# Kernel tuning notes

Measured on AMD Instinct MI355X. Metric: run time of the kernel, lower is better.

## Reference

```python
import jax, jax.numpy as jnp
import numpy as np

N = 50000
E = 800000
R = 5
D = 128
Q = D // 4  # 32


def setup_inputs() -> dict:
    key = jax.random.key(0)
    ks = jax.random.split(key, 24)
    s = 0.05
    inp = {
        'des': jax.random.normal(ks[0], (N, 768), jnp.float32),
        'tweet': jax.random.normal(ks[1], (N, 768), jnp.float32),
        'num_prop': jax.random.normal(ks[2], (N, 6), jnp.float32),
        'cat_prop': jax.random.normal(ks[3], (N, 11), jnp.float32),
        'edge_index': jax.random.randint(ks[4], (2, E), 0, N, dtype=jnp.int32),
        'edge_type': jax.random.randint(ks[5], (E,), 0, R, dtype=jnp.int32),
        'W_des': jax.random.normal(ks[6], (768, Q), jnp.float32) * s,
        'b_des': jnp.zeros((Q,), jnp.float32),
        'W_tw': jax.random.normal(ks[7], (768, Q), jnp.float32) * s,
        'b_tw': jnp.zeros((Q,), jnp.float32),
        'W_np': jax.random.normal(ks[8], (6, Q), jnp.float32) * s,
        'b_np': jnp.zeros((Q,), jnp.float32),
        'W_cp': jax.random.normal(ks[9], (11, Q), jnp.float32) * s,
        'b_cp': jnp.zeros((Q,), jnp.float32),
        'W_in': jax.random.normal(ks[10], (D, D), jnp.float32) * s,
        'b_in': jnp.zeros((D,), jnp.float32),
        'rel_w': jax.random.normal(ks[11], (R, D, D), jnp.float32) * s,
        'root_w': jax.random.normal(ks[12], (D, D), jnp.float32) * s,
        'rgcn_b': jnp.zeros((D,), jnp.float32),
        'W_o1': jax.random.normal(ks[13], (D, D), jnp.float32) * s,
        'b_o1': jnp.zeros((D,), jnp.float32),
        'W_o2': jax.random.normal(ks[14], (D, 2), jnp.float32) * s,
        'b_o2': jnp.zeros((2,), jnp.float32),
    }
    return inp


def _lrelu(v):
    return jax.nn.leaky_relu(v, negative_slope=0.01)


def _rgcn(x, edge_index, edge_type, rel_w, root_w, rgcn_b):
    # PyG RGCNConv with default mean aggregation per relation.
    n = x.shape[0]
    src, dst = edge_index[0], edge_index[1]
    h = jnp.einsum('nd,rde->rne', x, rel_w)          # [R, N, D]
    msg = h[edge_type, src]                          # [E, D] gather per edge
    seg = dst * R + edge_type                        # combined (node, relation) key
    sums = jax.ops.segment_sum(msg, seg, num_segments=n * R).reshape(n, R, -1)
    cnt = jax.ops.segment_sum(jnp.ones(msg.shape[0], jnp.float32), seg,
                              num_segments=n * R).reshape(n, R, 1)
    agg = (sums / jnp.maximum(cnt, 1.0)).sum(axis=1)  # mean per relation, sum over relations
    return agg + x @ root_w + rgcn_b


def reference(des, tweet, num_prop, cat_prop, edge_index, edge_type,
              W_des, b_des, W_tw, b_tw, W_np, b_np, W_cp, b_cp,
              W_in, b_in, rel_w, root_w, rgcn_b, W_o1, b_o1, W_o2, b_o2):
    d = _lrelu(des @ W_des + b_des)
    t = _lrelu(tweet @ W_tw + b_tw)
    n_ = _lrelu(num_prop @ W_np + b_np)
    c = _lrelu(cat_prop @ W_cp + b_cp)
    x = jnp.concatenate([d, t, n_, c], axis=1)       # [N, D]
    x = _lrelu(x @ W_in + b_in)
    for _ in range(4):
        x = _rgcn(x, edge_index, edge_type, rel_w, root_w, rgcn_b)
    x = _lrelu(x @ W_o1 + b_o1)
    return x @ W_o2 + b_o2                            # [N, 2]
```

## Files before the change

kernel.cpp:

```cpp
#include <hip/hip_runtime.h>


#define N_NODES 50000
#define N_EDGES 800000
#define R_REL   5
#define NSEG    (N_NODES * R_REL)
#define SCAN_BS 1024
#define SCAN_NB ((NSEG + SCAN_BS - 1) / SCAN_BS)

typedef __attribute__((ext_vector_type(8))) short bf16x8;
typedef __attribute__((ext_vector_type(4))) float f32x4;

__device__ __forceinline__ float lrelu(float v) { return v > 0.f ? v : 0.01f * v; }

__device__ __forceinline__ unsigned short f2bf_rne(float f) {
    unsigned u = __float_as_uint(f);
    return (unsigned short)((u + 0x7fff + ((u >> 16) & 1)) >> 16);
}

__device__ __forceinline__ void split1(float f, short& h, short& l) {
    unsigned u = __float_as_uint(f);
    unsigned short hh = (unsigned short)(u >> 16);
    h = (short)hh;
    l = (short)f2bf_rne(f - __uint_as_float((unsigned)hh << 16));
}

__device__ __forceinline__ void split8(const float* f, bf16x8& hi, bf16x8& lo) {
#pragma unroll
    for (int i = 0; i < 8; i++) {
        short h, l;
        split1(f[i], h, l);
        hi[i] = h;
        lo[i] = l;
    }
}

__global__ __launch_bounds__(256) void count_kernel(const int* __restrict__ ei,
                                                    const int* __restrict__ et,
                                                    int* __restrict__ cnt) {
    int e = blockIdx.x * 256 + threadIdx.x;
    if (e >= N_EDGES) return;
    atomicAdd(&cnt[ei[N_EDGES + e] * R_REL + et[e]], 1);
}

__global__ __launch_bounds__(SCAN_BS) void scan1(const int* __restrict__ cnt,
                                                 int* __restrict__ rowptr,
                                                 int* __restrict__ blockSums) {
    __shared__ int s[SCAN_BS];
    int t = threadIdx.x;
    int i = blockIdx.x * SCAN_BS + t;
    int v = (i < NSEG) ? cnt[i] : 0;
    s[t] = v;
    __syncthreads();
#pragma unroll
    for (int off = 1; off < SCAN_BS; off <<= 1) {
        int add = (t >= off) ? s[t - off] : 0;
        __syncthreads();
        s[t] += add;
        __syncthreads();
    }
    if (i < NSEG) rowptr[i] = s[t] - v;
    if (t == SCAN_BS - 1) blockSums[blockIdx.x] = s[t];
}

__global__ __launch_bounds__(256) void scan2(int* __restrict__ blockSums) {
    __shared__ int s[256];
    int t = threadIdx.x;
    int v = (t < SCAN_NB) ? blockSums[t] : 0;
    s[t] = v;
    __syncthreads();
#pragma unroll
    for (int off = 1; off < 256; off <<= 1) {
        int add = (t >= off) ? s[t - off] : 0;
        __syncthreads();
        s[t] += add;
        __syncthreads();
    }
    if (t < SCAN_NB) blockSums[t] = s[t] - v;
}

__global__ __launch_bounds__(SCAN_BS) void scan3(int* __restrict__ rowptr,
                                                 const int* __restrict__ blockSums) {
    int i = blockIdx.x * SCAN_BS + threadIdx.x;
    if (i == 0) rowptr[NSEG] = N_EDGES;
    if (i < NSEG) rowptr[i] += blockSums[blockIdx.x];
}

__global__ __launch_bounds__(256) void fill_kernel(const int* __restrict__ ei,
                                                   const int* __restrict__ et,
                                                   const int* __restrict__ rowptr,
                                                   int* __restrict__ cursor,
                                                   int* __restrict__ srcSorted) {
    int e = blockIdx.x * 256 + threadIdx.x;
    if (e >= N_EDGES) return;
    int seg = ei[N_EDGES + e] * R_REL + et[e];
    int pos = atomicAdd(&cursor[seg], 1);
    srcSorted[rowptr[seg] + pos] = ei[e];
}

__global__ __launch_bounds__(256) void build_bswz(const float* __restrict__ W,
                                                  int K, int NC, int NTILES,
                                                  short* __restrict__ out) {
    int tid = blockIdx.x * 256 + threadIdx.x;
    int total = (K / 32) * NTILES * 64;
    if (tid >= total) return;
    int l  = tid & 63;
    int nt = (tid >> 6) % NTILES;
    int c  = tid / (64 * NTILES);
    int n = nt * 16 + (l & 15);
    int k0 = c * 32 + (l >> 4) * 8;
    float f[8];
#pragma unroll
    for (int j = 0; j < 8; j++) f[j] = W[(size_t)(k0 + j) * NC + n];
    bf16x8 hi, lo;
    split8(f, hi, lo);
    size_t base = (size_t)c * (2 * NTILES * 512);
    *(bf16x8*)(out + base + ((size_t)nt * 64 + l) * 8) = hi;
    *(bf16x8*)(out + base + (size_t)NTILES * 512 + ((size_t)nt * 64 + l) * 8) = lo;
}

__global__ __launch_bounds__(256, 5) void rgcn_fused(const float* __restrict__ xf,
                                                     const int* __restrict__ rowptr,
                                                     const int* __restrict__ srcSorted,
                                                     const short* __restrict__ bz,
                                                     const float* __restrict__ rgcn_b,
                                                     float* __restrict__ xn, int M) {
    __shared__ short AhS[4][2048];
    __shared__ short AlS[4][2048];
    const int t = threadIdx.x;
    const int m0 = blockIdx.x * 64;
    const int w = t >> 6, l = t & 63;
    const int q = l >> 4, ln = l & 15;
    const int mw = w >> 1, nw = w & 1;
    const int rr = w * 16 + (t & 15);
    const int qq = (t >> 4) & 3;
    const int node = m0 + rr;
    const int sidx = w * 512 + l * 8;

    f32x4 acc[2][4];
#pragma unroll
    for (int mt = 0; mt < 2; mt++)
#pragma unroll
        for (int nt = 0; nt < 4; nt++) acc[mt][nt] = (f32x4)0.f;

    auto AGG = [&](int rel) {
        float ag[4][8];
#pragma unroll
        for (int c = 0; c < 4; c++)
#pragma unroll
            for (int j = 0; j < 8; j++) ag[c][j] = 0.f;
        int beg = 0, end = 0;
        if (node < M) {
            int s = node * R_REL + rel;
            beg = rowptr[s];
            end = rowptr[s + 1];
        }
        int i = beg;
        for (; i + 1 < end; i += 2) {
            int s0 = srcSorted[i];
            int s1 = srcSorted[i + 1];
            const float* p0 = xf + (size_t)s0 * 128 + qq * 8;
            const float* p1 = xf + (size_t)s1 * 128 + qq * 8;
#pragma unroll
            for (int c = 0; c < 4; c++) {
                float4 a0 = *(const float4*)(p0 + c * 32);
                float4 a1 = *(const float4*)(p0 + c * 32 + 4);
                float4 b0 = *(const float4*)(p1 + c * 32);
                float4 b1 = *(const float4*)(p1 + c * 32 + 4);
                ag[c][0] += a0.x + b0.x; ag[c][1] += a0.y + b0.y;
                ag[c][2] += a0.z + b0.z; ag[c][3] += a0.w + b0.w;
                ag[c][4] += a1.x + b1.x; ag[c][5] += a1.y + b1.y;
                ag[c][6] += a1.z + b1.z; ag[c][7] += a1.w + b1.w;
            }
        }
        if (i < end) {
            int s0 = srcSorted[i];
            const float* p0 = xf + (size_t)s0 * 128 + qq * 8;
#pragma unroll
            for (int c = 0; c < 4; c++) {
                float4 a0 = *(const float4*)(p0 + c * 32);
                float4 a1 = *(const float4*)(p0 + c * 32 + 4);
                ag[c][0] += a0.x; ag[c][1] += a0.y; ag[c][2] += a0.z; ag[c][3] += a0.w;
                ag[c][4] += a1.x; ag[c][5] += a1.y; ag[c][6] += a1.z; ag[c][7] += a1.w;
            }
        }
        int cnum = end - beg;
        float inv = cnum > 0 ? 1.f / (float)cnum : 0.f;
#pragma unroll
        for (int c = 0; c < 4; c++) {
            bf16x8 hv, lv;
#pragma unroll
            for (int j = 0; j < 8; j++) {
                short hh, ll;
                split1(ag[c][j] * inv, hh, ll);
                hv[j] = hh; lv[j] = ll;
            }
            *(bf16x8*)&AhS[c][sidx] = hv;
            *(bf16x8*)&AlS[c][sidx] = lv;
        }
    };

    auto ROOT = [&]() {
        int gr = node < M ? node : M - 1;
        const float* p0 = xf + (size_t)gr * 128 + qq * 8;
#pragma unroll
        for (int c = 0; c < 4; c++) {
            float f[8];
            *(float4*)&f[0] = *(const float4*)(p0 + c * 32);
            *(float4*)&f[4] = *(const float4*)(p0 + c * 32 + 4);
            bf16x8 hv, lv;
            split8(f, hv, lv);
            *(bf16x8*)&AhS[c][sidx] = hv;
            *(bf16x8*)&AlS[c][sidx] = lv;
        }
    };

    auto GEMMP = [&](const short* bzr) {
        bf16x8 BH[2][4], BL[2][4];
#pragma unroll
        for (int nt = 0; nt < 4; nt++) {
            const short* bp = bzr + (nw * 4 + nt) * 512 + l * 8;
            BH[0][nt] = *(const bf16x8*)(bp);
            BL[0][nt] = *(const bf16x8*)(bp + 4096);
        }
#pragma unroll
        for (int c = 0; c < 4; c++) {
            if (c < 3) {
#pragma unroll
                for (int nt = 0; nt < 4; nt++) {
                    const short* bp = bzr + (c + 1) * 8192 + (nw * 4 + nt) * 512 + l * 8;
                    BH[(c + 1) & 1][nt] = *(const bf16x8*)(bp);
                    BL[(c + 1) & 1][nt] = *(const bf16x8*)(bp + 4096);
                }
            }
            bf16x8 ah[2], al[2];
#pragma unroll
            for (int mt = 0; mt < 2; mt++) {
                ah[mt] = *(const bf16x8*)&AhS[c][(mw * 2 + mt) * 512 + l * 8];
                al[mt] = *(const bf16x8*)&AlS[c][(mw * 2 + mt) * 512 + l * 8];
            }
#pragma unroll
            for (int nt = 0; nt < 4; nt++) {
                bf16x8 bh = BH[c & 1][nt];
                bf16x8 bl2 = BL[c & 1][nt];
#pragma unroll
                for (int mt = 0; mt < 2; mt++) {
                    acc[mt][nt] = __builtin_amdgcn_mfma_f32_16x16x32_bf16(ah[mt], bh, acc[mt][nt], 0, 0, 0);
                    acc[mt][nt] = __builtin_amdgcn_mfma_f32_16x16x32_bf16(ah[mt], bl2, acc[mt][nt], 0, 0, 0);
                    acc[mt][nt] = __builtin_amdgcn_mfma_f32_16x16x32_bf16(al[mt], bh, acc[mt][nt], 0, 0, 0);
                }
            }
        }
    };

#pragma unroll 1
    for (int r = 0; r < 6; r++) {
        if (r > 0) __syncthreads();
        if (r < 5) AGG(r); else ROOT();
        __syncthreads();
        GEMMP(bz + (size_t)r * 32768);
    }

#pragma unroll
    for (int nt = 0; nt < 4; nt++) {
        int col = (nw * 4 + nt) * 16 + ln;
        float bv = rgcn_b[col];
#pragma unroll
        for (int mt = 0; mt < 2; mt++) {
            f32x4 v = acc[mt][nt];
#pragma unroll
            for (int i = 0; i < 4; i++) {
                int m = m0 + (mw * 2 + mt) * 16 + q * 4 + i;
                if (m < M) xn[(size_t)m * 128 + col] = v[i] + bv;
            }
        }
    }
}

template <int NT, bool ACT>
__global__ __launch_bounds__(256) void mfma_gemm(const float* __restrict__ A, int K,
                                                 const short* __restrict__ Bswz,
                                                 const float* __restrict__ bias,
                                                 float* __restrict__ C, int M,
                                                 int colofs) {
    constexpr int NH = NT / 2;
    __shared__ short Ahi[2048], Alo[2048];
    __shared__ short Bs[NT * 1024];
    const int t = threadIdx.x;
    const int m0 = blockIdx.x * 64;
    const int w = t >> 6, l = t & 63;
    const int q = l >> 4, ln = l & 15;
    const int mw = w >> 1, nw = w & 1;

    f32x4 acc[2][NH];
#pragma unroll
    for (int mt = 0; mt < 2; mt++)
#pragma unroll
        for (int nt = 0; nt < NH; nt++) acc[mt][nt] = (f32x4)0.f;

    const int nchunks = K / 32;
    const int r = t >> 2, qq = t & 3;
    const int aidx = (r >> 4) * 512 + qq * 128 + (r & 15) * 8;
    int gr = m0 + r; if (gr >= M) gr = M - 1;

    for (int c = 0; c < nchunks; c++) {
        __syncthreads();
        {
            const float* ap = A + (size_t)gr * K + c * 32 + qq * 8;
            float f[8];
            *(float4*)&f[0] = ((const float4*)ap)[0];
            *(float4*)&f[4] = ((const float4*)ap)[1];
            bf16x8 h0, l0;
            split8(f, h0, l0);
            *(bf16x8*)&Ahi[aidx] = h0;
            *(bf16x8*)&Alo[aidx] = l0;
        }
        {
            const short* gb = Bswz + (size_t)c * (NT * 1024);
#pragma unroll
            for (int i = 0; i < NH; i++) {
                int idx = i * 256 + t;
                *(bf16x8*)&Bs[idx * 8] = *(const bf16x8*)(gb + (size_t)idx * 8);
            }
        }
        __syncthreads();

        bf16x8 a_hi[2], a_lo[2];
#pragma unroll
        for (int mt = 0; mt < 2; mt++) {
            a_hi[mt] = *(const bf16x8*)&Ahi[(mw * 2 + mt) * 512 + l * 8];
            a_lo[mt] = *(const bf16x8*)&Alo[(mw * 2 + mt) * 512 + l * 8];
        }
#pragma unroll
        for (int nt = 0; nt < NH; nt++) {
            int ng = nw * NH + nt;
            bf16x8 bh = *(const bf16x8*)&Bs[(ng * 64 + l) * 8];
            bf16x8 bl = *(const bf16x8*)&Bs[NT * 512 + (ng * 64 + l) * 8];
#pragma unroll
            for (int mt = 0; mt < 2; mt++) {
                acc[mt][nt] = __builtin_amdgcn_mfma_f32_16x16x32_bf16(a_hi[mt], bh, acc[mt][nt], 0, 0, 0);
                acc[mt][nt] = __builtin_amdgcn_mfma_f32_16x16x32_bf16(a_hi[mt], bl, acc[mt][nt], 0, 0, 0);
                acc[mt][nt] = __builtin_amdgcn_mfma_f32_16x16x32_bf16(a_lo[mt], bh, acc[mt][nt], 0, 0, 0);
            }
        }
    }

#pragma unroll
    for (int nt = 0; nt < NH; nt++) {
        int ng = nw * NH + nt;
        int col = colofs + ng * 16 + ln;
        float bv = bias[ng * 16 + ln];
#pragma unroll
        for (int mt = 0; mt < 2; mt++) {
            f32x4 v = acc[mt][nt];
#pragma unroll
            for (int i = 0; i < 4; i++) {
                int m = m0 + (mw * 2 + mt) * 16 + q * 4 + i;
                if (m < M) {
                    float xv = v[i] + bv;
                    if (ACT) xv = lrelu(xv);
                    C[(size_t)m * 128 + col] = xv;
                }
            }
        }
    }
}

__global__ __launch_bounds__(256) void encode_small(const float* __restrict__ num_prop,
                                                    const float* __restrict__ cat_prop,
                                                    const float* __restrict__ W_np,
                                                    const float* __restrict__ b_np,
                                                    const float* __restrict__ W_cp,
                                                    const float* __restrict__ b_cp,
                                                    float* __restrict__ x) {
    int t = blockIdx.x * 256 + threadIdx.x;
    int node = t >> 6;
    int jj = t & 63;
    if (node >= N_NODES) return;
    if (jj < 32) {
        float acc = b_np[jj];
        const float* row = num_prop + (size_t)node * 6;
#pragma unroll
        for (int k = 0; k < 6; k++) acc = fmaf(row[k], W_np[k * 32 + jj], acc);
        x[(size_t)node * 128 + 64 + jj] = lrelu(acc);
    } else {
        int j = jj - 32;
        float acc = b_cp[j];
        const float* row = cat_prop + (size_t)node * 11;
#pragma unroll
        for (int k = 0; k < 11; k++) acc = fmaf(row[k], W_cp[k * 32 + j], acc);
        x[(size_t)node * 128 + 96 + j] = lrelu(acc);
    }
}

__global__ __launch_bounds__(256) void out_proj(const float* __restrict__ X,
                                                const float* __restrict__ W,
                                                const float* __restrict__ b,
                                                float* __restrict__ out, int M) {
    int n = blockIdx.x * 256 + threadIdx.x;
    if (n >= M) return;
    float a0 = b[0], a1 = b[1];
    const float4* xr = (const float4*)(X + (size_t)n * 128);
#pragma unroll
    for (int k4 = 0; k4 < 32; k4++) {
        float4 v = xr[k4];
        a0 = fmaf(v.x, W[(k4 * 4 + 0) * 2 + 0], a0);
        a1 = fmaf(v.x, W[(k4 * 4 + 0) * 2 + 1], a1);
        a0 = fmaf(v.y, W[(k4 * 4 + 1) * 2 + 0], a0);
        a1 = fmaf(v.y, W[(k4 * 4 + 1) * 2 + 1], a1);
        a0 = fmaf(v.z, W[(k4 * 4 + 2) * 2 + 0], a0);
        a1 = fmaf(v.z, W[(k4 * 4 + 2) * 2 + 1], a1);
        a0 = fmaf(v.w, W[(k4 * 4 + 3) * 2 + 0], a0);
        a1 = fmaf(v.w, W[(k4 * 4 + 3) * 2 + 1], a1);
    }
    out[(size_t)n * 2 + 0] = a0;
    out[(size_t)n * 2 + 1] = a1;
}

static inline size_t align64(size_t x) { return (x + 63) & ~(size_t)63; }

extern "C" void kernel_launch(void* const* d_in, const int* in_sizes, int n_in,
                              void* d_out, int out_size, void* d_ws, size_t ws_size,
                              hipStream_t stream) {
    const float* des      = (const float*)d_in[0];
    const float* tweet    = (const float*)d_in[1];
    const float* num_prop = (const float*)d_in[2];
    const float* cat_prop = (const float*)d_in[3];
    const int*   edge_index = (const int*)d_in[4];
    const int*   edge_type  = (const int*)d_in[5];
    const float* W_des = (const float*)d_in[6];  const float* b_des = (const float*)d_in[7];
    const float* W_tw  = (const float*)d_in[8];  const float* b_tw  = (const float*)d_in[9];
    const float* W_np  = (const float*)d_in[10]; const float* b_np  = (const float*)d_in[11];
    const float* W_cp  = (const float*)d_in[12]; const float* b_cp  = (const float*)d_in[13];
    const float* W_in  = (const float*)d_in[14]; const float* b_in  = (const float*)d_in[15];
    const float* rel_w = (const float*)d_in[16]; const float* root_w = (const float*)d_in[17];
    const float* rgcn_b = (const float*)d_in[18];
    const float* W_o1  = (const float*)d_in[19]; const float* b_o1  = (const float*)d_in[20];
    const float* W_o2  = (const float*)d_in[21]; const float* b_o2  = (const float*)d_in[22];
    float* out = (float*)d_out;

    char* p = (char*)d_ws;
    float* xA  = (float*)p;            p += (size_t)N_NODES * 128 * 4;
    float* xB  = (float*)p;            p += (size_t)N_NODES * 128 * 4;
    int* cnt       = (int*)p;          p += (size_t)NSEG * 4;
    int* rowptr    = (int*)p;          p += (size_t)(NSEG + 1) * 4;
    int* cursor    = (int*)p;          p += (size_t)NSEG * 4;
    int* srcSorted = (int*)p;          p += (size_t)N_EDGES * 4;
    int* blockSums = (int*)p;          p += (size_t)256 * 4;
    p = (char*)align64((size_t)p);
    short* bz_cat = (short*)p;         p += (size_t)6 * 32768 * 2;
    short* bz_in  = (short*)p;         p += (size_t)32768 * 2;
    short* bz_o1  = (short*)p;         p += (size_t)32768 * 2;
    short* bz_des = (short*)p;         p += (size_t)24 * 2048 * 2;
    short* bz_tw  = (short*)p;         p += (size_t)24 * 2048 * 2;

    for (int r = 0; r < R_REL; r++)
        build_bswz<<<8, 256, 0, stream>>>(rel_w + (size_t)r * 128 * 128, 128, 128, 8,
                                          bz_cat + (size_t)r * 32768);
    build_bswz<<<8, 256, 0, stream>>>(root_w, 128, 128, 8, bz_cat + (size_t)5 * 32768);
    build_bswz<<<8, 256, 0, stream>>>(W_in, 128, 128, 8, bz_in);
    build_bswz<<<8, 256, 0, stream>>>(W_o1, 128, 128, 8, bz_o1);
    build_bswz<<<12, 256, 0, stream>>>(W_des, 768, 32, 2, bz_des);
    build_bswz<<<12, 256, 0, stream>>>(W_tw, 768, 32, 2, bz_tw);

    hipMemsetAsync(cnt, 0, (size_t)NSEG * sizeof(int), stream);
    hipMemsetAsync(cursor, 0, (size_t)NSEG * sizeof(int), stream);
    count_kernel<<<(N_EDGES + 255) / 256, 256, 0, stream>>>(edge_index, edge_type, cnt);
    scan1<<<SCAN_NB, SCAN_BS, 0, stream>>>(cnt, rowptr, blockSums);
    scan2<<<1, 256, 0, stream>>>(blockSums);
    scan3<<<SCAN_NB, SCAN_BS, 0, stream>>>(rowptr, blockSums);
    fill_kernel<<<(N_EDGES + 255) / 256, 256, 0, stream>>>(
        edge_index, edge_type, rowptr, cursor, srcSorted);

    const int gm = (N_NODES + 63) / 64;

    encode_small<<<(N_NODES * 64 + 255) / 256, 256, 0, stream>>>(
        num_prop, cat_prop, W_np, b_np, W_cp, b_cp, xA);
    mfma_gemm<2, true><<<gm, 256, 0, stream>>>(des, 768, bz_des, b_des, xA, N_NODES, 0);
    mfma_gemm<2, true><<<gm, 256, 0, stream>>>(tweet, 768, bz_tw, b_tw, xA, N_NODES, 32);

    mfma_gemm<8, true><<<gm, 256, 0, stream>>>(xA, 128, bz_in, b_in, xB, N_NODES, 0);

    float* cur = xB; float* nxt = xA;
    for (int lyr = 0; lyr < 4; lyr++) {
        rgcn_fused<<<gm, 256, 0, stream>>>(cur, rowptr, srcSorted, bz_cat, rgcn_b, nxt, N_NODES);
        float* tmp = cur; cur = nxt; nxt = tmp;
    }

    mfma_gemm<8, true><<<gm, 256, 0, stream>>>(cur, 128, bz_o1, b_o1, nxt, N_NODES, 0);
    out_proj<<<(N_NODES + 255) / 256, 256, 0, stream>>>(nxt, W_o2, b_o2, out, N_NODES);
}
```

Measured before the change: 1.042 ms.

## Halve RGCN node tile to 32 and stage output through shared memory

```diff
diff --git a/kernel.cpp b/kernel.cpp
--- a/kernel.cpp
+++ b/kernel.cpp
@@ -119,36 +119,48 @@
     *(bf16x8*)(out + base + (size_t)NTILES * 512 + ((size_t)nt * 64 + l) * 8) = lo;
 }
 
-__global__ __launch_bounds__(256, 5) void rgcn_fused(const float* __restrict__ xf,
+__global__ __launch_bounds__(256, 6) void rgcn_fused(const float* __restrict__ xf,
                                                      const int* __restrict__ rowptr,
                                                      const int* __restrict__ srcSorted,
                                                      const short* __restrict__ bz,
                                                      const float* __restrict__ rgcn_b,
                                                      float* __restrict__ xn, int M) {
-    __shared__ short AhS[4][2048];
-    __shared__ short AlS[4][2048];
+    __shared__ __align__(16) char smem[16384];
+    short* AhS = (short*)smem;
+    short* AlS = (short*)(smem + 8192);
+    float* Co  = (float*)smem;
+
     const int t = threadIdx.x;
-    const int m0 = blockIdx.x * 64;
+    const int m0 = blockIdx.x * 32;
     const int w = t >> 6, l = t & 63;
     const int q = l >> 4, ln = l & 15;
     const int mw = w >> 1, nw = w & 1;
-    const int rr = w * 16 + (t & 15);
-    const int qq = (t >> 4) & 3;
+
+    const int rr = t & 31;
+    const int q8 = t >> 5;
     const int node = m0 + rr;
-    const int sidx = w * 512 + l * 8;
-
-    f32x4 acc[2][4];
-#pragma unroll
-    for (int mt = 0; mt < 2; mt++)
-#pragma unroll
-        for (int nt = 0; nt < 4; nt++) acc[mt][nt] = (f32x4)0.f;
+    const int cch = q8 >> 1;
+    const int kq0 = (q8 & 1) * 2;
+    const int sidx = cch * 1024 + (rr >> 4) * 512 + (kq0 * 16 + (rr & 15)) * 8;
+
+    f32x4 acc[4];
+#pragma unroll
+    for (int nt = 0; nt < 4; nt++) acc[nt] = (f32x4)0.f;
+
+    auto STAGE = [&](const float* ag) {
+        bf16x8 hv, lv;
+        split8(ag, hv, lv);
+        *(bf16x8*)&AhS[sidx] = hv;
+        *(bf16x8*)&AlS[sidx] = lv;
+        split8(ag + 8, hv, lv);
+        *(bf16x8*)&AhS[sidx + 128] = hv;
+        *(bf16x8*)&AlS[sidx + 128] = lv;
+    };
 
     auto AGG = [&](int rel) {
-        float ag[4][8];
-#pragma unroll
-        for (int c = 0; c < 4; c++)
-#pragma unroll
-            for (int j = 0; j < 8; j++) ag[c][j] = 0.f;
+        float ag[16];
+#pragma unroll
+        for (int j = 0; j < 16; j++) ag[j] = 0.f;
         int beg = 0, end = 0;
         if (node < M) {
             int s = node * R_REL + rel;
@@ -157,98 +169,60 @@
         }
         int i = beg;
         for (; i + 1 < end; i += 2) {
-            int s0 = srcSorted[i];
-            int s1 = srcSorted[i + 1];
-            const float* p0 = xf + (size_t)s0 * 128 + qq * 8;
-            const float* p1 = xf + (size_t)s1 * 128 + qq * 8;
-#pragma unroll
-            for (int c = 0; c < 4; c++) {
-                float4 a0 = *(const float4*)(p0 + c * 32);
-                float4 a1 = *(const float4*)(p0 + c * 32 + 4);
-                float4 b0 = *(const float4*)(p1 + c * 32);
-                float4 b1 = *(const float4*)(p1 + c * 32 + 4);
-                ag[c][0] += a0.x + b0.x; ag[c][1] += a0.y + b0.y;
-                ag[c][2] += a0.z + b0.z; ag[c][3] += a0.w + b0.w;
-                ag[c][4] += a1.x + b1.x; ag[c][5] += a1.y + b1.y;
-                ag[c][6] += a1.z + b1.z; ag[c][7] += a1.w + b1.w;
+            int s0 = srcSorted[i], s1 = srcSorted[i + 1];
+            const float4* p0 = (const float4*)(xf + (size_t)s0 * 128 + q8 * 16);
+            const float4* p1 = (const float4*)(xf + (size_t)s1 * 128 + q8 * 16);
+#pragma unroll
+            for (int c4 = 0; c4 < 4; c4++) {
+                float4 a = p0[c4], b = p1[c4];
+                ag[c4 * 4 + 0] += a.x + b.x; ag[c4 * 4 + 1] += a.y + b.y;
+                ag[c4 * 4 + 2] += a.z + b.z; ag[c4 * 4 + 3] += a.w + b.w;
             }
         }
         if (i < end) {
             int s0 = srcSorted[i];
-            const float* p0 = xf + (size_t)s0 * 128 + qq * 8;
-#pragma unroll
-            for (int c = 0; c < 4; c++) {
-                float4 a0 = *(const float4*)(p0 + c * 32);
-                float4 a1 = *(const float4*)(p0 + c * 32 + 4);
-                ag[c][0] += a0.x; ag[c][1] += a0.y; ag[c][2] += a0.z; ag[c][3] += a0.w;
-                ag[c][4] += a1.x; ag[c][5] += a1.y; ag[c][6] += a1.z; ag[c][7] += a1.w;
+            const float4* p0 = (const float4*)(xf + (size_t)s0 * 128 + q8 * 16);
+#pragma unroll
+            for (int c4 = 0; c4 < 4; c4++) {
+                float4 a = p0[c4];
+                ag[c4 * 4 + 0] += a.x; ag[c4 * 4 + 1] += a.y;
+                ag[c4 * 4 + 2] += a.z; ag[c4 * 4 + 3] += a.w;
             }
         }
         int cnum = end - beg;
         float inv = cnum > 0 ? 1.f / (float)cnum : 0.f;
 #pragma unroll
-        for (int c = 0; c < 4; c++) {
-            bf16x8 hv, lv;
-#pragma unroll
-            for (int j = 0; j < 8; j++) {
-                short hh, ll;
-                split1(ag[c][j] * inv, hh, ll);
-                hv[j] = hh; lv[j] = ll;
-            }
-            *(bf16x8*)&AhS[c][sidx] = hv;
-            *(bf16x8*)&AlS[c][sidx] = lv;
-        }
+        for (int j = 0; j < 16; j++) ag[j] *= inv;
+        STAGE(ag);
     };
 
     auto ROOT = [&]() {
         int gr = node < M ? node : M - 1;
-        const float* p0 = xf + (size_t)gr * 128 + qq * 8;
+        float ag[16];
+        const float4* p0 = (const float4*)(xf + (size_t)gr * 128 + q8 * 16);
+#pragma unroll
+        for (int c4 = 0; c4 < 4; c4++) {
+            float4 a = p0[c4];
+            ag[c4 * 4 + 0] = a.x; ag[c4 * 4 + 1] = a.y;
+            ag[c4 * 4 + 2] = a.z; ag[c4 * 4 + 3] = a.w;
+        }
+        STAGE(ag);
+    };
+
+    auto GEMMP = [&](const short* bzr) {
 #pragma unroll
         for (int c = 0; c < 4; c++) {
-            float f[8];
-            *(float4*)&f[0] = *(const float4*)(p0 + c * 32);
-            *(float4*)&f[4] = *(const float4*)(p0 + c * 32 + 4);
-            bf16x8 hv, lv;
-            split8(f, hv, lv);
-            *(bf16x8*)&AhS[c][sidx] = hv;
-            *(bf16x8*)&AlS[c][sidx] = lv;
-        }
-    };
-
-    auto GEMMP = [&](const short* bzr) {
-        bf16x8 BH[2][4], BL[2][4];
-#pragma unroll
-        for (int nt = 0; nt < 4; nt++) {
-            const short* bp = bzr + (nw * 4 + nt) * 512 + l * 8;
-            BH[0][nt] = *(const bf16x8*)(bp);
-            BL[0][nt] = *(const bf16x8*)(bp + 4096);
-        }
-#pragma unroll
-        for (int c = 0; c < 4; c++) {
-            if (c < 3) {
-#pragma unroll
-                for (int nt = 0; nt < 4; nt++) {
-                    const short* bp = bzr + (c + 1) * 8192 + (nw * 4 + nt) * 512 + l * 8;
-                    BH[(c + 1) & 1][nt] = *(const bf16x8*)(bp);
-                    BL[(c + 1) & 1][nt] = *(const bf16x8*)(bp + 4096);
-                }
-            }
-            bf16x8 ah[2], al[2];
-#pragma unroll
-            for (int mt = 0; mt < 2; mt++) {
-                ah[mt] = *(const bf16x8*)&AhS[c][(mw * 2 + mt) * 512 + l * 8];
-                al[mt] = *(const bf16x8*)&AlS[c][(mw * 2 + mt) * 512 + l * 8];
-            }
+            bf16x8 ah = *(const bf16x8*)&AhS[c * 1024 + mw * 512 + l * 8];
+            bf16x8 al = *(const bf16x8*)&AlS[c * 1024 + mw * 512 + l * 8];
 #pragma unroll
             for (int nt = 0; nt < 4; nt++) {
-                bf16x8 bh = BH[c & 1][nt];
-                bf16x8 bl2 = BL[c & 1][nt];
-#pragma unroll
-                for (int mt = 0; mt < 2; mt++) {
-                    acc[mt][nt] = __builtin_amdgcn_mfma_f32_16x16x32_bf16(ah[mt], bh, acc[mt][nt], 0, 0, 0);
-                    acc[mt][nt] = __builtin_amdgcn_mfma_f32_16x16x32_bf16(ah[mt], bl2, acc[mt][nt], 0, 0, 0);
-                    acc[mt][nt] = __builtin_amdgcn_mfma_f32_16x16x32_bf16(al[mt], bh, acc[mt][nt], 0, 0, 0);
-                }
+                int ng = nw * 4 + nt;
+                const short* bp = bzr + c * 8192 + ng * 512 + l * 8;
+                bf16x8 bh = *(const bf16x8*)(bp);
+                bf16x8 bl2 = *(const bf16x8*)(bp + 4096);
+                acc[nt] = __builtin_amdgcn_mfma_f32_16x16x32_bf16(ah, bh, acc[nt], 0, 0, 0);
+                acc[nt] = __builtin_amdgcn_mfma_f32_16x16x32_bf16(ah, bl2, acc[nt], 0, 0, 0);
+                acc[nt] = __builtin_amdgcn_mfma_f32_16x16x32_bf16(al, bh, acc[nt], 0, 0, 0);
             }
         }
     };
@@ -261,19 +235,26 @@
         GEMMP(bz + (size_t)r * 32768);
     }
 
+    __syncthreads();
 #pragma unroll
     for (int nt = 0; nt < 4; nt++) {
         int col = (nw * 4 + nt) * 16 + ln;
         float bv = rgcn_b[col];
-#pragma unroll
-        for (int mt = 0; mt < 2; mt++) {
-            f32x4 v = acc[mt][nt];
-#pragma unroll
-            for (int i = 0; i < 4; i++) {
-                int m = m0 + (mw * 2 + mt) * 16 + q * 4 + i;
-                if (m < M) xn[(size_t)m * 128 + col] = v[i] + bv;
-            }
-        }
+        f32x4 v = acc[nt];
+#pragma unroll
+        for (int i = 0; i < 4; i++) {
+            int row = mw * 16 + q * 4 + i;
+            Co[row * 128 + col] = v[i] + bv;
+        }
+    }
+    __syncthreads();
+#pragma unroll
+    for (int it = 0; it < 4; it++) {
+        int idx = it * 256 + t;
+        int row = idx >> 5, c4 = idx & 31;
+        int m = m0 + row;
+        if (m < M)
+            ((float4*)(xn + (size_t)m * 128))[c4] = ((const float4*)(Co + row * 128))[c4];
     }
 }
 
@@ -473,6 +454,7 @@
         edge_index, edge_type, rowptr, cursor, srcSorted);
 
     const int gm = (N_NODES + 63) / 64;
+    const int gm32 = (N_NODES + 31) / 32;
 
     encode_small<<<(N_NODES * 64 + 255) / 256, 256, 0, stream>>>(
         num_prop, cat_prop, W_np, b_np, W_cp, b_cp, xA);
@@ -483,7 +465,7 @@
 
     float* cur = xB; float* nxt = xA;
     for (int lyr = 0; lyr < 4; lyr++) {
-        rgcn_fused<<<gm, 256, 0, stream>>>(cur, rowptr, srcSorted, bz_cat, rgcn_b, nxt, N_NODES);
+        rgcn_fused<<<gm32, 256, 0, stream>>>(cur, rowptr, srcSorted, bz_cat, rgcn_b, nxt, N_NODES);
         float* tmp = cur; cur = nxt; nxt = tmp;
     }
 
```

Result: slower. 1.076 ms (+3.2%).
